# Performance work log

Hardware: AMD Instinct MI355X
Metric: run time of the kernel (lower is better)

## Reference

```python
import jax, jax.numpy as jnp
import numpy as np

HIDDEN = 512
HEADS = 8
HEAD_DIM = HIDDEN // HEADS
INNER = int(HIDDEN * 4.0)
MAX_DIST = 512
LN_EPS = 1e-5


def _layernorm(x, g, b):
    mu = jnp.mean(x, axis=-1, keepdims=True)
    var = jnp.var(x, axis=-1, keepdims=True)
    return (x - mu) * jax.lax.rsqrt(var + LN_EPS) * g + b


def setup_inputs() -> dict:
    key = jax.random.key(0)
    ks = jax.random.split(key, 12)
    B, T = 4, 2048
    s = 0.02
    return {
        "x": jax.random.normal(ks[0], (B, T, HIDDEN), dtype=jnp.float32),
        "w_qkv": jax.random.normal(ks[1], (HIDDEN, 3 * HIDDEN), dtype=jnp.float32) * s,
        "b_qkv": jnp.zeros((3 * HIDDEN,), dtype=jnp.float32),
        "w_out": jax.random.normal(ks[2], (HIDDEN, HIDDEN), dtype=jnp.float32) * s,
        "b_out": jnp.zeros((HIDDEN,), dtype=jnp.float32),
        "ln1_g": jnp.ones((HIDDEN,), dtype=jnp.float32),
        "ln1_b": jnp.zeros((HIDDEN,), dtype=jnp.float32),
        "ln2_g": jnp.ones((HIDDEN,), dtype=jnp.float32),
        "ln2_b": jnp.zeros((HIDDEN,), dtype=jnp.float32),
        "w_mlp1": jax.random.normal(ks[3], (HIDDEN, INNER), dtype=jnp.float32) * s,
        "b_mlp1": jnp.zeros((INNER,), dtype=jnp.float32),
        "w_mlp2": jax.random.normal(ks[4], (INNER, HIDDEN), dtype=jnp.float32) * s,
        "b_mlp2": jnp.zeros((HIDDEN,), dtype=jnp.float32),
        "rel_table": jax.random.normal(ks[5], (2 * MAX_DIST + 1, HEADS), dtype=jnp.float32) * s,
    }


def reference(x, w_qkv, b_qkv, w_out, b_out, ln1_g, ln1_b, ln2_g, ln2_b,
              w_mlp1, b_mlp1, w_mlp2, b_mlp2, rel_table):
    B, T, C = x.shape
    scale = HEAD_DIM ** -0.5
    qkv = x @ w_qkv + b_qkv  # [B,T,3C]
    qkv = qkv.reshape(B, T, 3, HEADS, HEAD_DIM)
    q = qkv[:, :, 0].transpose(0, 2, 1, 3)  # [B,H,T,D]
    k = qkv[:, :, 1].transpose(0, 2, 1, 3)
    v = qkv[:, :, 2].transpose(0, 2, 1, 3)
    logits = jnp.einsum('bhqd,bhkd->bhqk', q, k) * scale
    # relative position bias: clamp(q_pos - k_pos) lookup -> [H,T,T]
    rel = jnp.clip(jnp.arange(T)[:, None] - jnp.arange(T)[None, :], -MAX_DIST, MAX_DIST) + MAX_DIST
    bias = rel_table[rel].transpose(2, 0, 1)  # [H,T,T]
    logits = logits + bias[None]
    attn = jax.nn.softmax(logits, axis=-1)
    out = jnp.einsum('bhqk,bhkd->bhqd', attn, v)
    out = out.transpose(0, 2, 1, 3).reshape(B, T, C)
    out = out @ w_out + b_out
    x = _layernorm(x + out, ln1_g, ln1_b)
    h = jax.nn.gelu(x @ w_mlp1 + b_mlp1, approximate=False)
    mlp_out = h @ w_mlp2 + b_mlp2
    return _layernorm(x + mlp_out, ln2_g, ln2_b)
```

## Files before the change

### kernel.cpp

```cpp
#include <hip/hip_runtime.h>
#include <hip/hip_bf16.h>

using bf16 = __hip_bfloat16;
typedef __attribute__((ext_vector_type(8))) short bf16x8;
typedef __attribute__((ext_vector_type(4))) short bf16x4;
typedef __attribute__((ext_vector_type(4))) float f32x4;

#define HIDDEN 512
#define HEADS 8
#define HDIM 64
#define INNER 2048
#define MAXD 512
#define BB 4
#define TT 2048
#define MM (BB*TT)
#define LOG2E 1.44269504088896340736f

typedef const __attribute__((address_space(1))) unsigned int* gas_u32p;
typedef __attribute__((address_space(3))) unsigned int* las_u32p;

__device__ __forceinline__ void gload_lds16(const void* g, void* l) {
    __builtin_amdgcn_global_load_lds((gas_u32p)g, (las_u32p)l, 16, 0, 0);
}
__device__ __forceinline__ short bfr(float x) {
    return (short)__bfloat16_as_ushort(__float2bfloat16(x));
}

__global__ __launch_bounds__(256) void cast_kernel(const float* __restrict__ in,
                                                   bf16* __restrict__ out) {
    int i = (blockIdx.x * 256 + threadIdx.x) * 4;
    float4 v = *(const float4*)&in[i];
    bf16 o[4] = {__float2bfloat16(v.x), __float2bfloat16(v.y),
                 __float2bfloat16(v.z), __float2bfloat16(v.w)};
    *(bf16x4*)&out[i] = *(bf16x4*)o;
}

__global__ __launch_bounds__(256) void wtrans_kernel(const float* __restrict__ in,
                                                     bf16* __restrict__ out,
                                                     int K, int N) {
    __shared__ float tile[32][33];
    int bx = blockIdx.x;
    int by = blockIdx.y;
    int lx = threadIdx.x & 31, ly = threadIdx.x >> 5;
    #pragma unroll
    for (int i = 0; i < 4; ++i)
        tile[ly + 8*i][lx] = in[(size_t)(by*32 + ly + 8*i) * N + bx*32 + lx];
    __syncthreads();
    #pragma unroll
    for (int i = 0; i < 4; ++i)
        out[(size_t)(bx*32 + ly + 8*i) * K + by*32 + lx] =
            __float2bfloat16(tile[lx][ly + 8*i]);
}

template<int EPI, int BN, int VT, int RESID>
__global__ __launch_bounds__(256) void gemm_kernel(
    const bf16* __restrict__ A, const bf16* __restrict__ BT,
    const float* __restrict__ bias, const float* __restrict__ resid,
    void* __restrict__ C, bf16* __restrict__ vt_out,
    int M, int N, int K)
{
    constexpr int NBF = BN / 32;
    constexpr int BBYTES = BN * 64;
    __shared__ __align__(16) bf16 As[2][128*32];
    __shared__ __align__(16) bf16 Bs[2][BN*32];
    const int tid = threadIdx.x;
    const int wid = tid >> 6;
    const int lane = tid & 63;
    const int lhi = lane >> 4, llo = lane & 15;
    const int m0 = blockIdx.x * 128, n0 = blockIdx.y * BN;
    const int wr = wid >> 1, wc = wid & 1;

    const int srow = tid >> 2;
    const int scol = ((tid & 3) ^ ((srow >> 1) & 3)) * 8;
    const bf16* Ap = A + (size_t)(m0 + srow) * K + scol;
    const bf16* Bp = BT + (size_t)(n0 + srow) * K + scol;
    const size_t step64 = (size_t)64 * K;
    const int rsw = (llo >> 1) & 3;

    f32x4 acc[4][NBF] = {};

    gload_lds16(Ap,          (char*)As + tid*16);
    gload_lds16(Ap + step64, (char*)As + 4096 + tid*16);
    gload_lds16(Bp,          (char*)Bs + tid*16);
    if (BN == 128) gload_lds16(Bp + step64, (char*)Bs + 4096 + tid*16);

    const int NK = K >> 5;
    for (int it = 0; it < NK; ++it) {
        const int p = it & 1;
        __syncthreads();
        if (it + 1 < NK) {
            const int k1 = (it + 1) << 5;
            gload_lds16(Ap + k1,          (char*)As + (p^1)*8192 + tid*16);
            gload_lds16(Ap + k1 + step64, (char*)As + (p^1)*8192 + 4096 + tid*16);
            gload_lds16(Bp + k1,          (char*)Bs + (p^1)*BBYTES + tid*16);
            if (BN == 128) gload_lds16(Bp + k1 + step64, (char*)Bs + (p^1)*BBYTES + 4096 + tid*16);
        }
        bf16x8 af[4], bfrg[NBF];
        #pragma unroll
        for (int ar = 0; ar < 4; ++ar)
            af[ar] = *(const bf16x8*)((const char*)As + p*8192 +
                       (64*wr + 16*ar + llo)*64 + ((lhi ^ rsw) << 4));
        #pragma unroll
        for (int bc = 0; bc < NBF; ++bc)
            bfrg[bc] = *(const bf16x8*)((const char*)Bs + p*BBYTES +
                       ((BN/2)*wc + 16*bc + llo)*64 + ((lhi ^ rsw) << 4));
        #pragma unroll
        for (int ar = 0; ar < 4; ++ar)
            #pragma unroll
            for (int bc = 0; bc < NBF; ++bc)
                acc[ar][bc] = __builtin_amdgcn_mfma_f32_16x16x32_bf16(
                    af[ar], bfrg[bc], acc[ar][bc], 0, 0, 0);
    }

    if (VT && n0 >= 1024) {
        #pragma unroll
        for (int ar = 0; ar < 4; ++ar) {
            const int row = m0 + 64*wr + 16*ar + 4*lhi;
            const int bq = row >> 11, t0 = row & 2047;
            #pragma unroll
            for (int bc = 0; bc < NBF; ++bc) {
                const int cv = n0 - 1024 + (BN/2)*wc + 16*bc + llo;
                const int h = cv >> 6, d = cv & 63;
                float bv = bias[n0 + (BN/2)*wc + 16*bc + llo];
                bf16x4 pk = {bfr(acc[ar][bc][0] + bv), bfr(acc[ar][bc][1] + bv),
                             bfr(acc[ar][bc][2] + bv), bfr(acc[ar][bc][3] + bv)};
                *(bf16x4*)&vt_out[(((size_t)(bq*8 + h) * 64 + d) << 11) + t0] = pk;
            }
        }
        return;
    }

    #pragma unroll
    for (int ar = 0; ar < 4; ++ar) {
        #pragma unroll
        for (int j = 0; j < 4; ++j) {
            int row = m0 + 64*wr + 16*ar + 4*lhi + j;
            #pragma unroll
            for (int bc = 0; bc < NBF; ++bc) {
                int col = n0 + (BN/2)*wc + 16*bc + llo;
                float v = acc[ar][bc][j] + bias[col];
                if (RESID) v += resid[(size_t)row * N + col];
                if (EPI == 2) {
                    float u = 0.7978845608028654f * (v + 0.044715f * v * v * v);
                    float e = __builtin_amdgcn_exp2f(u * (2.0f * LOG2E));
                    v = v * (1.0f - 1.0f / (1.0f + e));
                }
                if (EPI == 1)
                    ((float*)C)[(size_t)row * N + col] = v;
                else
                    ((bf16*)C)[(size_t)row * N + col] = __float2bfloat16(v);
            }
        }
    }
}

#define PTN (TT + 128)
__global__ __launch_bounds__(512) void attn_kernel(
    const bf16* __restrict__ qkv,
    const bf16* __restrict__ v_t,
    const float* __restrict__ rel_table,
    bf16* __restrict__ attn_out)
{
    __shared__ __align__(16) bf16 Ks[2][64*64];
    __shared__ __align__(16) bf16 Vs[2][64*64];
    __shared__ __align__(16) bf16 Ps[8][16*64];
    __shared__ float PT[PTN];

    const int qt = blockIdx.x, bh = blockIdx.y;
    const int b = bh >> 3, h = bh & 7;
    const int tid = threadIdx.x, wid = tid >> 6, lane = tid & 63;
    const int lhi = lane >> 4, llo = lane & 15;

    const int lo = qt * 128 - (TT - 1);
    for (int i = tid; i < PTN; i += 512) {
        int idx = min(max(i + lo, -MAXD), MAXD) + MAXD;
        PT[i] = rel_table[(size_t)idx * HEADS + h] * LOG2E;
    }

    const int q0w = qt * 128 + wid * 16;
    const int qb = qt * 128;
    const int q = q0w + llo;
    bf16x8 bq[2];
    #pragma unroll
    for (int kc = 0; kc < 2; ++kc)
        bq[kc] = *(const bf16x8*)&qkv[(size_t)(b*TT + q) * 1536 + h*64 + kc*32 + lhi*8];

    const int so = tid * 16;
    const int r0 = so >> 7;
    const int c0 = (((so & 127) ^ ((r0 & 7) << 4)) >> 1);
    const bf16* kbase = qkv + (size_t)(b*TT) * 1536 + 512 + h*64;
    const bf16* vbase = v_t + (size_t)bh * 64 * TT;

    float accL = 0.f;
    f32x4 accO[4] = {};
    const int pti = wid*16 + llo + (TT - 1);

    gload_lds16(kbase + (size_t)r0 * 1536 + c0, (char*)Ks + so);
    gload_lds16(vbase + (size_t)r0 * TT + c0,   (char*)Vs + so);
    __syncthreads();

    const float cFut  = PT[min(max(-512 - lo, 0), PTN - 1)];
    const float cPast = PT[min(max( 512 - lo, 0), PTN - 1)];

    constexpr int NT = TT / 64;
    for (int kt = 0; kt < NT; ++kt) {
        const int p = kt & 1;
        const int kv0 = kt * 64;
        if (kt) __syncthreads();
        if (kt + 1 < NT) {
            const int kn = kv0 + 64;
            gload_lds16(kbase + (size_t)(kn + r0) * 1536 + c0, (char*)Ks + (p^1)*8192 + so);
            gload_lds16(vbase + (size_t)r0 * TT + kn + c0,     (char*)Vs + (p^1)*8192 + so);
        }
        const char* Kb = (const char*)Ks + p*8192;
        const char* Vb = (const char*)Vs + p*8192;

        f32x4 s[4];
        __builtin_amdgcn_s_setprio(1);
        #pragma unroll
        for (int f = 0; f < 4; ++f) {
            f32x4 a = {};
            const int rr = 16*f + llo;
            #pragma unroll
            for (int kc = 0; kc < 2; ++kc) {
                bf16x8 ak = *(const bf16x8*)(Kb + rr*128 + (((4*kc + lhi) ^ (rr & 7)) << 4));
                a = __builtin_amdgcn_mfma_f32_16x16x32_bf16(ak, bq[kc], a, 0, 0, 0);
            }
            s[f] = a;
        }
        __builtin_amdgcn_s_setprio(0);

        const float sc = 0.125f * LOG2E;
        if (kv0 >= qb + 640) {
            #pragma unroll
            for (int f = 0; f < 4; ++f)
                #pragma unroll
                for (int j = 0; j < 4; ++j)
                    s[f][j] = fmaf(s[f][j], sc, cFut);
        } else if (kv0 + 576 <= qb) {
            #pragma unroll
            for (int f = 0; f < 4; ++f)
                #pragma unroll
                for (int j = 0; j < 4; ++j)
                    s[f][j] = fmaf(s[f][j], sc, cPast);
        } else {
            const int ib = pti - kv0;
            #pragma unroll
            for (int f = 0; f < 4; ++f)
                #pragma unroll
                for (int j = 0; j < 4; ++j)
                    s[f][j] = fmaf(s[f][j], sc, PT[ib - 16*f - 4*lhi - j]);
        }

        float tf[4];
        #pragma unroll
        for (int f = 0; f < 4; ++f) {
            float p0 = __builtin_amdgcn_exp2f(s[f][0]);
            float p1 = __builtin_amdgcn_exp2f(s[f][1]);
            float p2 = __builtin_amdgcn_exp2f(s[f][2]);
            float p3 = __builtin_amdgcn_exp2f(s[f][3]);
            tf[f] = (p0 + p1) + (p2 + p3);
            bf16x4 pk = {bfr(p0), bfr(p1), bfr(p2), bfr(p3)};
            *(bf16x4*)((char*)Ps + wid*2048 + llo*128 +
                       ((f*32 + lhi*8) ^ ((llo & 7) << 4))) = pk;
        }
        accL += (tf[0] + tf[1]) + (tf[2] + tf[3]);

        bf16x8 pf[2];
        #pragma unroll
        for (int kc = 0; kc < 2; ++kc)
            pf[kc] = *(const bf16x8*)((const char*)Ps + wid*2048 + llo*128 +
                                      ((kc*64 + lhi*16) ^ ((llo & 7) << 4)));
        __builtin_amdgcn_s_setprio(1);
        #pragma unroll
        for (int kc = 0; kc < 2; ++kc)
            #pragma unroll
            for (int f = 0; f < 4; ++f) {
                const int rr = 16*f + llo;
                bf16x8 av = *(const bf16x8*)(Vb + rr*128 + (((4*kc + lhi) ^ (rr & 7)) << 4));
                accO[f] = __builtin_amdgcn_mfma_f32_16x16x32_bf16(av, pf[kc], accO[f], 0, 0, 0);
            }
        __builtin_amdgcn_s_setprio(0);
    }

    accL += __shfl_xor(accL, 16, 64);
    accL += __shfl_xor(accL, 32, 64);
    const float rl = 1.0f / accL;
    const int row = b*TT + q;
    #pragma unroll
    for (int f = 0; f < 4; ++f) {
        bf16x4 ov = {bfr(accO[f][0] * rl), bfr(accO[f][1] * rl),
                     bfr(accO[f][2] * rl), bfr(accO[f][3] * rl)};
        *(bf16x4*)&attn_out[(size_t)row * HIDDEN + h*64 + 16*f + 4*lhi] = ov;
    }
}

template<int WB>
__global__ __launch_bounds__(256) void ln_kernel(
    const float* __restrict__ in,
    const float* __restrict__ g, const float* __restrict__ bb,
    float* __restrict__ of, bf16* __restrict__ ob)
{
    int row = blockIdx.x * 4 + (threadIdx.x >> 6);
    int lane = threadIdx.x & 63;
    const float* pa = in + (size_t)row * HIDDEN;
    float v[8];
    float s = 0.f, sq = 0.f;
    #pragma unroll
    for (int i = 0; i < 2; ++i) {
        float4 a4 = *(const float4*)&pa[lane*4 + i*256];
        v[i*4+0] = a4.x; v[i*4+1] = a4.y; v[i*4+2] = a4.z; v[i*4+3] = a4.w;
        #pragma unroll
        for (int j = 0; j < 4; ++j) { s += v[i*4+j]; sq += v[i*4+j]*v[i*4+j]; }
    }
    #pragma unroll
    for (int d = 1; d < 64; d <<= 1) {
        s  += __shfl_xor(s,  d, 64);
        sq += __shfl_xor(sq, d, 64);
    }
    float mean = s * (1.f / HIDDEN);
    float var  = sq * (1.f / HIDDEN) - mean * mean;
    float rstd = rsqrtf(var + 1e-5f);
    #pragma unroll
    for (int i = 0; i < 2; ++i)
        #pragma unroll
        for (int j = 0; j < 4; ++j) {
            int col = lane*4 + i*256 + j;
            float o = (v[i*4+j] - mean) * rstd * g[col] + bb[col];
            of[(size_t)row * HIDDEN + col] = o;
            if (WB) ob[(size_t)row * HIDDEN + col] = __float2bfloat16(o);
        }
}

extern "C" void kernel_launch(void* const* d_in, const int* in_sizes, int n_in,
                              void* d_out, int out_size, void* d_ws, size_t ws_size,
                              hipStream_t stream) {
    const float* x     = (const float*)d_in[0];
    const float* w_qkv = (const float*)d_in[1];
    const float* b_qkv = (const float*)d_in[2];
    const float* w_out = (const float*)d_in[3];
    const float* b_out = (const float*)d_in[4];
    const float* ln1_g = (const float*)d_in[5];
    const float* ln1_b = (const float*)d_in[6];
    const float* ln2_g = (const float*)d_in[7];
    const float* ln2_b = (const float*)d_in[8];
    const float* w1    = (const float*)d_in[9];
    const float* b1    = (const float*)d_in[10];
    const float* w2    = (const float*)d_in[11];
    const float* b2    = (const float*)d_in[12];
    const float* rel   = (const float*)d_in[13];
    float* out = (float*)d_out;

    char* ws = (char*)d_ws;
    bf16*  xb     = (bf16*)(ws + 0);
    bf16*  wqkv_t = (bf16*)(ws + 8388608);
    bf16*  wout_t = (bf16*)(ws + 9961472);
    bf16*  w1_t   = (bf16*)(ws + 10485760);
    bf16*  w2_t   = (bf16*)(ws + 12582912);
    bf16*  qkv    = (bf16*)(ws + 14680064);
    bf16*  v_t    = (bf16*)(ws + 39845888);
    bf16*  attn_o = (bf16*)(ws + 48234496);
    float* proj   = (float*)(ws + 56623104);
    float* x1     = (float*)(ws + 73400320);
    bf16*  h      = (bf16*)(ws + 14680064);
    bf16*  x1b    = (bf16*)(ws + 90177536);

    cast_kernel<<<MM*HIDDEN/4/256, 256, 0, stream>>>(x, xb);
    wtrans_kernel<<<dim3(1536/32, 512/32),  256, 0, stream>>>(w_qkv, wqkv_t, 512, 1536);
    wtrans_kernel<<<dim3(512/32,  512/32),  256, 0, stream>>>(w_out, wout_t, 512, 512);
    wtrans_kernel<<<dim3(2048/32, 512/32),  256, 0, stream>>>(w1,    w1_t,   512, 2048);
    wtrans_kernel<<<dim3(512/32,  2048/32), 256, 0, stream>>>(w2,    w2_t,   2048, 512);
    gemm_kernel<0,128,1,0><<<dim3(MM/128, 1536/128), 256, 0, stream>>>(
        xb, wqkv_t, b_qkv, nullptr, qkv, v_t, MM, 1536, 512);
    attn_kernel<<<dim3(TT/128, BB*HEADS), 512, 0, stream>>>(qkv, v_t, rel, attn_o);
    gemm_kernel<1,64,0,1><<<dim3(MM/128, 512/64), 256, 0, stream>>>(
        attn_o, wout_t, b_out, x, proj, nullptr, MM, 512, 512);
    ln_kernel<1><<<MM/4, 256, 0, stream>>>(proj, ln1_g, ln1_b, x1, x1b);
    gemm_kernel<2,128,0,0><<<dim3(MM/128, 2048/128), 256, 0, stream>>>(
        x1b, w1_t, b1, nullptr, h, nullptr, MM, 2048, 512);
    gemm_kernel<1,64,0,1><<<dim3(MM/128, 512/64), 256, 0, stream>>>(
        h, w2_t, b2, x1, proj, nullptr, MM, 512, 2048);
    ln_kernel<0><<<MM/4, 256, 0, stream>>>(proj, ln2_g, ln2_b, out, nullptr);
}
```

Baseline: 191.8 us.

## Use bf16 intermediates, add 64x64 GEMM for N=512 projections, bf16 bias table

Narrows the projection outputs and the LN1 result from fp32 to bf16, so the fp32 x1 buffer goes away and the second residual reads the bf16 x1b. Adds a smaller 64x64-tile GEMM for the N=512 projections, giving more blocks in flight, and vectorises the layernorm loads and stores. The attention bias table in shared memory becomes bf16. This cuts memory traffic and improves occupancy, at the cost of lower precision in residuals and bias values.

```diff
diff --git a/kernel.cpp b/kernel.cpp
--- a/kernel.cpp
+++ b/kernel.cpp
@@ -25,6 +25,9 @@
 __device__ __forceinline__ short bfr(float x) {
     return (short)__bfloat16_as_ushort(__float2bfloat16(x));
 }
+__device__ __forceinline__ float bf2f(short u) {
+    return __uint_as_float(((unsigned)(unsigned short)u) << 16);
+}
 
 __global__ __launch_bounds__(256) void cast_kernel(const float* __restrict__ in,
                                                    bf16* __restrict__ out) {
@@ -52,10 +55,10 @@
             __float2bfloat16(tile[lx][ly + 8*i]);
 }
 
-template<int EPI, int BN, int VT, int RESID>
+template<int EPI, int BN, int VT>
 __global__ __launch_bounds__(256) void gemm_kernel(
     const bf16* __restrict__ A, const bf16* __restrict__ BT,
-    const float* __restrict__ bias, const float* __restrict__ resid,
+    const float* __restrict__ bias,
     void* __restrict__ C, bf16* __restrict__ vt_out,
     int M, int N, int K)
 {
@@ -139,16 +142,83 @@
             for (int bc = 0; bc < NBF; ++bc) {
                 int col = n0 + (BN/2)*wc + 16*bc + llo;
                 float v = acc[ar][bc][j] + bias[col];
-                if (RESID) v += resid[(size_t)row * N + col];
                 if (EPI == 2) {
                     float u = 0.7978845608028654f * (v + 0.044715f * v * v * v);
                     float e = __builtin_amdgcn_exp2f(u * (2.0f * LOG2E));
                     v = v * (1.0f - 1.0f / (1.0f + e));
                 }
-                if (EPI == 1)
-                    ((float*)C)[(size_t)row * N + col] = v;
-                else
-                    ((bf16*)C)[(size_t)row * N + col] = __float2bfloat16(v);
+                ((bf16*)C)[(size_t)row * N + col] = __float2bfloat16(v);
+            }
+        }
+    }
+}
+
+template<int RESID>
+__global__ __launch_bounds__(256) void gemm_small(
+    const bf16* __restrict__ A, const bf16* __restrict__ BT,
+    const float* __restrict__ bias, const void* __restrict__ resid,
+    bf16* __restrict__ C, int M, int N, int K)
+{
+    __shared__ __align__(16) bf16 As[2][64*32];
+    __shared__ __align__(16) bf16 Bs[2][64*32];
+    const int tid = threadIdx.x;
+    const int wid = tid >> 6;
+    const int lane = tid & 63;
+    const int lhi = lane >> 4, llo = lane & 15;
+    const int m0 = blockIdx.x * 64, n0 = blockIdx.y * 64;
+    const int wr = wid >> 1, wc = wid & 1;
+
+    const int srow = tid >> 2;
+    const int scol = ((tid & 3) ^ ((srow >> 1) & 3)) * 8;
+    const bf16* Ap = A + (size_t)(m0 + srow) * K + scol;
+    const bf16* Bp = BT + (size_t)(n0 + srow) * K + scol;
+    const int rsw = (llo >> 1) & 3;
+
+    f32x4 acc[2][2] = {};
+
+    gload_lds16(Ap, (char*)As + tid*16);
+    gload_lds16(Bp, (char*)Bs + tid*16);
+
+    const int NK = K >> 5;
+    for (int it = 0; it < NK; ++it) {
+        const int p = it & 1;
+        __syncthreads();
+        if (it + 1 < NK) {
+            const int k1 = (it + 1) << 5;
+            gload_lds16(Ap + k1, (char*)As + (p^1)*4096 + tid*16);
+            gload_lds16(Bp + k1, (char*)Bs + (p^1)*4096 + tid*16);
+        }
+        bf16x8 af[2], bfrg[2];
+        #pragma unroll
+        for (int ar = 0; ar < 2; ++ar)
+            af[ar] = *(const bf16x8*)((const char*)As + p*4096 +
+                       (32*wr + 16*ar + llo)*64 + ((lhi ^ rsw) << 4));
+        #pragma unroll
+        for (int bc = 0; bc < 2; ++bc)
+            bfrg[bc] = *(const bf16x8*)((const char*)Bs + p*4096 +
+                       (32*wc + 16*bc + llo)*64 + ((lhi ^ rsw) << 4));
+        #pragma unroll
+        for (int ar = 0; ar < 2; ++ar)
+            #pragma unroll
+            for (int bc = 0; bc < 2; ++bc)
+                acc[ar][bc] = __builtin_amdgcn_mfma_f32_16x16x32_bf16(
+                    af[ar], bfrg[bc], acc[ar][bc], 0, 0, 0);
+    }
+
+    #pragma unroll
+    for (int ar = 0; ar < 2; ++ar) {
+        #pragma unroll
+        for (int j = 0; j < 4; ++j) {
+            int row = m0 + 32*wr + 16*ar + 4*lhi + j;
+            #pragma unroll
+            for (int bc = 0; bc < 2; ++bc) {
+                int col = n0 + 32*wc + 16*bc + llo;
+                float v = acc[ar][bc][j] + bias[col];
+                if (RESID == 1)
+                    v += ((const float*)resid)[(size_t)row * N + col];
+                if (RESID == 2)
+                    v += __bfloat162float(((const bf16*)resid)[(size_t)row * N + col]);
+                C[(size_t)row * N + col] = __float2bfloat16(v);
             }
         }
     }
@@ -164,7 +234,7 @@
     __shared__ __align__(16) bf16 Ks[2][64*64];
     __shared__ __align__(16) bf16 Vs[2][64*64];
     __shared__ __align__(16) bf16 Ps[8][16*64];
-    __shared__ float PT[PTN];
+    __shared__ bf16 PT[PTN];
 
     const int qt = blockIdx.x, bh = blockIdx.y;
     const int b = bh >> 3, h = bh & 7;
@@ -174,7 +244,7 @@
     const int lo = qt * 128 - (TT - 1);
     for (int i = tid; i < PTN; i += 512) {
         int idx = min(max(i + lo, -MAXD), MAXD) + MAXD;
-        PT[i] = rel_table[(size_t)idx * HEADS + h] * LOG2E;
+        PT[i] = __float2bfloat16(rel_table[(size_t)idx * HEADS + h] * LOG2E);
     }
 
     const int q0w = qt * 128 + wid * 16;
@@ -199,8 +269,8 @@
     gload_lds16(vbase + (size_t)r0 * TT + c0,   (char*)Vs + so);
     __syncthreads();
 
-    const float cFut  = PT[min(max(-512 - lo, 0), PTN - 1)];
-    const float cPast = PT[min(max( 512 - lo, 0), PTN - 1)];
+    const float cFut  = __bfloat162float(PT[min(max(-512 - lo, 0), PTN - 1)]);
+    const float cPast = __bfloat162float(PT[min(max( 512 - lo, 0), PTN - 1)]);
 
     constexpr int NT = TT / 64;
     for (int kt = 0; kt < NT; ++kt) {
@@ -249,7 +319,7 @@
             for (int f = 0; f < 4; ++f)
                 #pragma unroll
                 for (int j = 0; j < 4; ++j)
-                    s[f][j] = fmaf(s[f][j], sc, PT[ib - 16*f - 4*lhi - j]);
+                    s[f][j] = fmaf(s[f][j], sc, __bfloat162float(PT[ib - 16*f - 4*lhi - j]));
         }
 
         float tf[4];
@@ -297,21 +367,20 @@
 
 template<int WB>
 __global__ __launch_bounds__(256) void ln_kernel(
-    const float* __restrict__ in,
+    const bf16* __restrict__ in,
     const float* __restrict__ g, const float* __restrict__ bb,
     float* __restrict__ of, bf16* __restrict__ ob)
 {
     int row = blockIdx.x * 4 + (threadIdx.x >> 6);
     int lane = threadIdx.x & 63;
-    const float* pa = in + (size_t)row * HIDDEN;
+    const bf16* pa = in + (size_t)row * HIDDEN + lane * 8;
+    bf16x8 v8 = *(const bf16x8*)pa;
     float v[8];
     float s = 0.f, sq = 0.f;
     #pragma unroll
-    for (int i = 0; i < 2; ++i) {
-        float4 a4 = *(const float4*)&pa[lane*4 + i*256];
-        v[i*4+0] = a4.x; v[i*4+1] = a4.y; v[i*4+2] = a4.z; v[i*4+3] = a4.w;
-        #pragma unroll
-        for (int j = 0; j < 4; ++j) { s += v[i*4+j]; sq += v[i*4+j]*v[i*4+j]; }
+    for (int j = 0; j < 8; ++j) {
+        v[j] = bf2f(v8[j]);
+        s += v[j]; sq += v[j] * v[j];
     }
     #pragma unroll
     for (int d = 1; d < 64; d <<= 1) {
@@ -321,15 +390,23 @@
     float mean = s * (1.f / HIDDEN);
     float var  = sq * (1.f / HIDDEN) - mean * mean;
     float rstd = rsqrtf(var + 1e-5f);
-    #pragma unroll
-    for (int i = 0; i < 2; ++i)
-        #pragma unroll
-        for (int j = 0; j < 4; ++j) {
-            int col = lane*4 + i*256 + j;
-            float o = (v[i*4+j] - mean) * rstd * g[col] + bb[col];
-            of[(size_t)row * HIDDEN + col] = o;
-            if (WB) ob[(size_t)row * HIDDEN + col] = __float2bfloat16(o);
-        }
+    float o[8];
+    #pragma unroll
+    for (int j = 0; j < 8; ++j) {
+        int col = lane * 8 + j;
+        o[j] = (v[j] - mean) * rstd * g[col] + bb[col];
+    }
+    if (WB) {
+        bf16x8 ov;
+        #pragma unroll
+        for (int j = 0; j < 8; ++j) ov[j] = bfr(o[j]);
+        *(bf16x8*)&ob[(size_t)row * HIDDEN + lane * 8] = ov;
+    } else {
+        float4 o0 = {o[0], o[1], o[2], o[3]};
+        float4 o1 = {o[4], o[5], o[6], o[7]};
+        *(float4*)&of[(size_t)row * HIDDEN + lane * 8]     = o0;
+        *(float4*)&of[(size_t)row * HIDDEN + lane * 8 + 4] = o1;
+    }
 }
 
 extern "C" void kernel_launch(void* const* d_in, const int* in_sizes, int n_in,
@@ -360,8 +437,7 @@
     bf16*  qkv    = (bf16*)(ws + 14680064);
     bf16*  v_t    = (bf16*)(ws + 39845888);
     bf16*  attn_o = (bf16*)(ws + 48234496);
-    float* proj   = (float*)(ws + 56623104);
-    float* x1     = (float*)(ws + 73400320);
+    bf16*  proj   = (bf16*)(ws + 56623104);
     bf16*  h      = (bf16*)(ws + 14680064);
     bf16*  x1b    = (bf16*)(ws + 90177536);
 
@@ -370,15 +446,15 @@
     wtrans_kernel<<<dim3(512/32,  512/32),  256, 0, stream>>>(w_out, wout_t, 512, 512);
     wtrans_kernel<<<dim3(2048/32, 512/32),  256, 0, stream>>>(w1,    w1_t,   512, 2048);
     wtrans_kernel<<<dim3(512/32,  2048/32), 256, 0, stream>>>(w2,    w2_t,   2048, 512);
-    gemm_kernel<0,128,1,0><<<dim3(MM/128, 1536/128), 256, 0, stream>>>(
-        xb, wqkv_t, b_qkv, nullptr, qkv, v_t, MM, 1536, 512);
+    gemm_kernel<0,128,1><<<dim3(MM/128, 1536/128), 256, 0, stream>>>(
+        xb, wqkv_t, b_qkv, qkv, v_t, MM, 1536, 512);
     attn_kernel<<<dim3(TT/128, BB*HEADS), 512, 0, stream>>>(qkv, v_t, rel, attn_o);
-    gemm_kernel<1,64,0,1><<<dim3(MM/128, 512/64), 256, 0, stream>>>(
-        attn_o, wout_t, b_out, x, proj, nullptr, MM, 512, 512);
-    ln_kernel<1><<<MM/4, 256, 0, stream>>>(proj, ln1_g, ln1_b, x1, x1b);
-    gemm_kernel<2,128,0,0><<<dim3(MM/128, 2048/128), 256, 0, stream>>>(
-        x1b, w1_t, b1, nullptr, h, nullptr, MM, 2048, 512);
-    gemm_kernel<1,64,0,1><<<dim3(MM/128, 512/64), 256, 0, stream>>>(
-        h, w2_t, b2, x1, proj, nullptr, MM, 512, 2048);
+    gemm_small<1><<<dim3(MM/64, 512/64), 256, 0, stream>>>(
+        attn_o, wout_t, b_out, x, proj, MM, 512, 512);
+    ln_kernel<1><<<MM/4, 256, 0, stream>>>(proj, ln1_g, ln1_b, nullptr, x1b);
+    gemm_kernel<2,128,0><<<dim3(MM/128, 2048/128), 256, 0, stream>>>(
+        x1b, w1_t, b1, h, nullptr, MM, 2048, 512);
+    gemm_small<2><<<dim3(MM/64, 512/64), 256, 0, stream>>>(
+        h, w2_t, b2, x1b, proj, MM, 512, 2048);
     ln_kernel<0><<<MM/4, 256, 0, stream>>>(proj, ln2_g, ln2_b, out, nullptr);
 }
```

Measured after the change: 211.3 us. 10.2% more time.
